# Performance work log

Hardware: AMD Instinct MI355X
Metric: run time of the kernel (lower is better)

Reference implementation:

```python
import jax, jax.numpy as jnp
import numpy as np

B, T, E = 2, 512, 1024        # batch, max_tokens, embedding dim
S, A = 2048, 30               # num_spans, max_arg_span


def setup_inputs() -> dict:
    key = jax.random.key(0)
    k1, k2, k3, k4 = jax.random.split(key, 4)
    x = jax.random.normal(k1, (B, T, E), dtype=jnp.float32)
    W = jax.random.normal(k2, (E, 1), dtype=jnp.float32) * (1.0 / np.sqrt(E))
    b = jnp.zeros((1,), dtype=jnp.float32)
    start = jax.random.randint(k3, (S,), 0, T, dtype=jnp.int32)
    width = jax.random.randint(k4, (S,), 1, A + 1, dtype=jnp.int32)
    end = jnp.minimum(start + width - 1, T - 1).astype(jnp.int32)
    return {"x": x, "W": W, "b": b, "start": start, "end": end}


def reference(x, W, b, start, end):
    # span_indices: clamp start+offset to last token, shape [S, A]
    span_idx = jnp.minimum(jnp.arange(A)[None, :] + start[:, None], T - 1)
    # gather span token embeddings: [B, S, A, E]
    span_emb = x[:, span_idx, :]
    # tiny per-token head score: Dense(1, relu) -> [B, T, 1]
    head_scores = jax.nn.relu(x @ W + b)
    # validity mask over span positions (log-mask), [S, A]
    span_width = end - start + 1
    valid = jnp.arange(A)[None, :] < span_width[:, None]
    log_mask = jnp.where(valid, 0.0, -jnp.inf)
    # gather scores per span position, add log-mask: [B, S, A, 1]
    span_head = head_scores[:, span_idx, :] + log_mask[None, :, :, None]
    # softmax over span-position axis (axis=2)
    attn = jax.nn.softmax(span_head, axis=2)
    # weighted-sum pooling over span positions -> [B, S, E]
    return jnp.sum(span_emb * attn, axis=2)
```

## Files before the change

### kernel.cpp

```cpp
#include <hip/hip_runtime.h>
#include <math.h>

#define TT 512
#define EE 1024
#define AA 30

typedef float f32x4 __attribute__((ext_vector_type(4)));

static __device__ __forceinline__ float dot4(f32x4 p, f32x4 q) {
    return p.x * q.x + p.y * q.y + p.z * q.z + p.w * q.w;
}

template <int SWZ>
__global__ __launch_bounds__(256) void fused_span_kernel(const float* __restrict__ x,
                                                         const float* __restrict__ W,
                                                         const float* __restrict__ bias,
                                                         const int* __restrict__ start,
                                                         const int* __restrict__ end,
                                                         float* __restrict__ out,
                                                         int S, int G) {
    int bid  = blockIdx.x;
    int wv   = threadIdx.x >> 6;
    int lane = threadIdx.x & 63;
    int b, s, g;
    if (SWZ) {
        int xcd = bid & 7;
        b = xcd >> 2;
        int local = ((bid >> 3) << 2) | (xcd & 3);
        s = local * 4 + wv;
        g = b * S + s;
    } else {
        g = bid * 4 + wv;
        if (g >= G) return;
        b = g / S;
        s = g - b * S;
    }

    int st = start[s];
    int nA = min(end[s] - st + 1, AA);

    const f32x4* xb = reinterpret_cast<const f32x4*>(x + ((size_t)b * TT + st) * EE) + lane;
    const f32x4* wp = reinterpret_cast<const f32x4*>(W) + lane;

    f32x4 w0 = wp[0], w1 = wp[64], w2 = wp[128], w3 = wp[192];
    f32x4 a0 = (f32x4)(0.f), a1 = (f32x4)(0.f), a2 = (f32x4)(0.f), a3 = (f32x4)(0.f);
    float sum = 0.f;
    float bsc = bias[0];

    int a = 0;
    for (; a + 2 <= nA; a += 2) {
        const f32x4* r0 = xb + (size_t)a * (EE / 4);
        const f32x4* r1 = r0 + (EE / 4);
        f32x4 v0 = r0[0], v1 = r0[64], v2 = r0[128], v3 = r0[192];
        f32x4 u0 = r1[0], u1 = r1[64], u2 = r1[128], u3 = r1[192];
        float d0 = dot4(v0, w0) + dot4(v1, w1) + dot4(v2, w2) + dot4(v3, w3);
        float d1 = dot4(u0, w0) + dot4(u1, w1) + dot4(u2, w2) + dot4(u3, w3);
        #pragma unroll
        for (int off = 32; off; off >>= 1) {
            d0 += __shfl_xor(d0, off, 64);
            d1 += __shfl_xor(d1, off, 64);
        }
        float p0 = __expf(fmaxf(d0 + bsc, 0.f));
        float p1 = __expf(fmaxf(d1 + bsc, 0.f));
        sum += p0 + p1;
        a0 += p0 * v0 + p1 * u0;
        a1 += p0 * v1 + p1 * u1;
        a2 += p0 * v2 + p1 * u2;
        a3 += p0 * v3 + p1 * u3;
    }
    if (a < nA) {
        const f32x4* r0 = xb + (size_t)a * (EE / 4);
        f32x4 v0 = r0[0], v1 = r0[64], v2 = r0[128], v3 = r0[192];
        float d0 = dot4(v0, w0) + dot4(v1, w1) + dot4(v2, w2) + dot4(v3, w3);
        #pragma unroll
        for (int off = 32; off; off >>= 1) d0 += __shfl_xor(d0, off, 64);
        float p0 = __expf(fmaxf(d0 + bsc, 0.f));
        sum += p0;
        a0 += p0 * v0;
        a1 += p0 * v1;
        a2 += p0 * v2;
        a3 += p0 * v3;
    }

    float inv = 1.0f / sum;
    f32x4* op = reinterpret_cast<f32x4*>(out + (size_t)g * EE) + lane;
    __builtin_nontemporal_store(a0 * inv, op);
    __builtin_nontemporal_store(a1 * inv, op + 64);
    __builtin_nontemporal_store(a2 * inv, op + 128);
    __builtin_nontemporal_store(a3 * inv, op + 192);
}

extern "C" void kernel_launch(void* const* d_in, const int* in_sizes, int n_in,
                              void* d_out, int out_size, void* d_ws, size_t ws_size,
                              hipStream_t stream) {
    const float* x     = (const float*)d_in[0];
    const float* W     = (const float*)d_in[1];
    const float* bias  = (const float*)d_in[2];
    const int*   start = (const int*)d_in[3];
    const int*   end   = (const int*)d_in[4];
    float*       out   = (float*)d_out;

    const int BT = in_sizes[0] / EE;
    const int S  = in_sizes[3];
    const int B  = BT / TT;
    const int G  = B * S;

    if (B == 2 && S == 2048) {
        fused_span_kernel<1><<<G / 4, 256, 0, stream>>>(x, W, bias, start, end, out, S, G);
    } else {
        fused_span_kernel<0><<<(G + 3) / 4, 256, 0, stream>>>(x, W, bias, start, end, out, S, G);
    }
}
```

Before: 19.55 us.

## Replace per-span weighted gather with chunked prefix sums and combine

Computes exp(relu(score)) per token once, builds chunk-local prefix sums of e*x over 32-token chunks plus chunk totals, and forms each span's weighted sum from at most three prefix rows. This removes the per-span loop over up to 30 token rows and their repeated dot products. In exchange it adds two extra kernel launches, writes a full prefix array to workspace, and relies on prefix subtraction, which can lose floating-point precision. The fused kernel remains as a fallback when workspace is too small.

```diff
diff --git a/kernel.cpp b/kernel.cpp
--- a/kernel.cpp
+++ b/kernel.cpp
@@ -4,11 +4,107 @@
 #define TT 512
 #define EE 1024
 #define AA 30
+#define CH 32
+#define NC (TT / CH)
 
 typedef float f32x4 __attribute__((ext_vector_type(4)));
 
 static __device__ __forceinline__ float dot4(f32x4 p, f32x4 q) {
     return p.x * q.x + p.y * q.y + p.z * q.z + p.w * q.w;
+}
+
+__global__ __launch_bounds__(256) void score_kernel(const float* __restrict__ x,
+                                                    const float* __restrict__ W,
+                                                    const float* __restrict__ bias,
+                                                    float* __restrict__ es, int BT) {
+    int row  = blockIdx.x * 4 + (threadIdx.x >> 6);
+    int lane = threadIdx.x & 63;
+    if (row >= BT) return;
+    const f32x4* xr = reinterpret_cast<const f32x4*>(x + (size_t)row * EE);
+    const f32x4* wr = reinterpret_cast<const f32x4*>(W);
+    float acc = 0.f;
+    #pragma unroll
+    for (int k = 0; k < 4; ++k) {
+        int i = lane + 64 * k;
+        acc += dot4(xr[i], wr[i]);
+    }
+    #pragma unroll
+    for (int off = 32; off; off >>= 1) acc += __shfl_xor(acc, off, 64);
+    if (lane == 0) es[row] = __expf(fmaxf(acc + bias[0], 0.0f));
+}
+
+__global__ __launch_bounds__(256) void prefix_kernel(const float* __restrict__ x,
+                                                     const float* __restrict__ es,
+                                                     float* __restrict__ Pp,
+                                                     float* __restrict__ C) {
+    int blk = blockIdx.x;
+    int b = blk / NC, tc = blk - b * NC;
+    int t0 = tc * CH;
+    size_t rowoff = ((size_t)b * TT + t0) * (EE / 4);
+    const f32x4* xb = reinterpret_cast<const f32x4*>(x) + rowoff + threadIdx.x;
+    f32x4*       pp = reinterpret_cast<f32x4*>(Pp)      + rowoff + threadIdx.x;
+    const float* e  = es + b * TT + t0;
+    f32x4 acc = (f32x4)(0.f);
+    #pragma unroll 8
+    for (int i = 0; i < CH; ++i) {
+        acc += e[i] * xb[(size_t)i * (EE / 4)];
+        pp[(size_t)i * (EE / 4)] = acc;
+    }
+    reinterpret_cast<f32x4*>(C)[((size_t)b * NC + tc) * (EE / 4) + threadIdx.x] = acc;
+}
+
+template <int SWZ>
+__global__ __launch_bounds__(256) void combine_kernel(const float* __restrict__ Pp,
+                                                      const float* __restrict__ C,
+                                                      const float* __restrict__ es,
+                                                      const int* __restrict__ start,
+                                                      const int* __restrict__ end,
+                                                      float* __restrict__ out,
+                                                      int S, int G) {
+    int bid  = blockIdx.x;
+    int wv   = threadIdx.x >> 6;
+    int lane = threadIdx.x & 63;
+    int b, s, g;
+    if (SWZ) {
+        int xcd = bid & 7;
+        b = xcd >> 2;
+        int local = ((bid >> 3) << 2) | (xcd & 3);
+        s = local * 4 + wv;
+        g = b * S + s;
+    } else {
+        g = bid * 4 + wv;
+        if (g >= G) return;
+        b = g / S;
+        s = g - b * S;
+    }
+
+    int st = start[s];
+    int nA = min(end[s] - st + 1, AA);
+    int en = st + nA - 1;
+
+    float ev = (lane < nA) ? es[b * TT + st + lane] : 0.f;
+    #pragma unroll
+    for (int off = 32; off; off >>= 1) ev += __shfl_xor(ev, off, 64);
+    float inv = 1.0f / ev;
+
+    const f32x4* base = reinterpret_cast<const f32x4*>(Pp + (size_t)b * TT * EE) + lane;
+    const f32x4* pe = base + (size_t)en * (EE / 4);
+    f32x4 n0 = pe[0], n1 = pe[64], n2 = pe[128], n3 = pe[192];
+    if (st & (CH - 1)) {
+        const f32x4* ps = base + (size_t)(st - 1) * (EE / 4);
+        n0 -= ps[0]; n1 -= ps[64]; n2 -= ps[128]; n3 -= ps[192];
+    }
+    int cs = st / CH, ce = en / CH;
+    if (ce > cs) {
+        const f32x4* pc = reinterpret_cast<const f32x4*>(C + ((size_t)b * NC + cs) * EE) + lane;
+        n0 += pc[0]; n1 += pc[64]; n2 += pc[128]; n3 += pc[192];
+    }
+
+    f32x4* op = reinterpret_cast<f32x4*>(out + (size_t)g * EE) + lane;
+    __builtin_nontemporal_store(n0 * inv, op);
+    __builtin_nontemporal_store(n1 * inv, op + 64);
+    __builtin_nontemporal_store(n2 * inv, op + 128);
+    __builtin_nontemporal_store(n3 * inv, op + 192);
 }
 
 template <int SWZ>
@@ -35,40 +131,14 @@
         b = g / S;
         s = g - b * S;
     }
-
     int st = start[s];
     int nA = min(end[s] - st + 1, AA);
-
     const f32x4* xb = reinterpret_cast<const f32x4*>(x + ((size_t)b * TT + st) * EE) + lane;
     const f32x4* wp = reinterpret_cast<const f32x4*>(W) + lane;
-
     f32x4 w0 = wp[0], w1 = wp[64], w2 = wp[128], w3 = wp[192];
     f32x4 a0 = (f32x4)(0.f), a1 = (f32x4)(0.f), a2 = (f32x4)(0.f), a3 = (f32x4)(0.f);
-    float sum = 0.f;
-    float bsc = bias[0];
-
-    int a = 0;
-    for (; a + 2 <= nA; a += 2) {
-        const f32x4* r0 = xb + (size_t)a * (EE / 4);
-        const f32x4* r1 = r0 + (EE / 4);
-        f32x4 v0 = r0[0], v1 = r0[64], v2 = r0[128], v3 = r0[192];
-        f32x4 u0 = r1[0], u1 = r1[64], u2 = r1[128], u3 = r1[192];
-        float d0 = dot4(v0, w0) + dot4(v1, w1) + dot4(v2, w2) + dot4(v3, w3);
-        float d1 = dot4(u0, w0) + dot4(u1, w1) + dot4(u2, w2) + dot4(u3, w3);
-        #pragma unroll
-        for (int off = 32; off; off >>= 1) {
-            d0 += __shfl_xor(d0, off, 64);
-            d1 += __shfl_xor(d1, off, 64);
-        }
-        float p0 = __expf(fmaxf(d0 + bsc, 0.f));
-        float p1 = __expf(fmaxf(d1 + bsc, 0.f));
-        sum += p0 + p1;
-        a0 += p0 * v0 + p1 * u0;
-        a1 += p0 * v1 + p1 * u1;
-        a2 += p0 * v2 + p1 * u2;
-        a3 += p0 * v3 + p1 * u3;
-    }
-    if (a < nA) {
+    float sum = 0.f, bsc = bias[0];
+    for (int a = 0; a < nA; ++a) {
         const f32x4* r0 = xb + (size_t)a * (EE / 4);
         f32x4 v0 = r0[0], v1 = r0[64], v2 = r0[128], v3 = r0[192];
         float d0 = dot4(v0, w0) + dot4(v1, w1) + dot4(v2, w2) + dot4(v3, w3);
@@ -76,12 +146,8 @@
         for (int off = 32; off; off >>= 1) d0 += __shfl_xor(d0, off, 64);
         float p0 = __expf(fmaxf(d0 + bsc, 0.f));
         sum += p0;
-        a0 += p0 * v0;
-        a1 += p0 * v1;
-        a2 += p0 * v2;
-        a3 += p0 * v3;
+        a0 += p0 * v0; a1 += p0 * v1; a2 += p0 * v2; a3 += p0 * v3;
     }
-
     float inv = 1.0f / sum;
     f32x4* op = reinterpret_cast<f32x4*>(out + (size_t)g * EE) + lane;
     __builtin_nontemporal_store(a0 * inv, op);
@@ -105,9 +171,23 @@
     const int B  = BT / TT;
     const int G  = B * S;
 
-    if (B == 2 && S == 2048) {
-        fused_span_kernel<1><<<G / 4, 256, 0, stream>>>(x, W, bias, start, end, out, S, G);
+    float* es = (float*)d_ws;
+    float* Pp = (float*)((char*)d_ws + 8192);
+    float* C  = (float*)((char*)d_ws + 8192 + (size_t)BT * EE * 4);
+    size_t need = 8192 + (size_t)BT * EE * 4 + (size_t)B * NC * EE * 4;
+
+    bool fast = (ws_size >= need) && (B * TT == BT) && (BT % 4 == 0);
+    if (fast) {
+        score_kernel<<<BT / 4, 256, 0, stream>>>(x, W, bias, es, BT);
+        prefix_kernel<<<B * NC, 256, 0, stream>>>(x, es, Pp, C);
+        if (B == 2 && S == 2048)
+            combine_kernel<1><<<G / 4, 256, 0, stream>>>(Pp, C, es, start, end, out, S, G);
+        else
+            combine_kernel<0><<<(G + 3) / 4, 256, 0, stream>>>(Pp, C, es, start, end, out, S, G);
     } else {
-        fused_span_kernel<0><<<(G + 3) / 4, 256, 0, stream>>>(x, W, bias, start, end, out, S, G);
+        if (B == 2 && S == 2048)
+            fused_span_kernel<1><<<G / 4, 256, 0, stream>>>(x, W, bias, start, end, out, S, G);
+        else
+            fused_span_kernel<0><<<(G + 3) / 4, 256, 0, stream>>>(x, W, bias, start, end, out, S, G);
     }
 }
```

Result: slower. 20.74 us (+6.1%).
